# Optimization experiments

Hardware: AMD Instinct MI355X
Metric: run time of the kernel (lower is better)

## Reference

```python
import jax, jax.numpy as jnp
import numpy as np

B, N, E, H = 32, 1024, 1024, 8
D = E // H      # head_dim = 128, att_mid_dim = [128, 64, 128]
MID = 64


def setup_inputs() -> dict:
    key = jax.random.key(0)
    ks = jax.random.split(key, 12)

    def lin(k, out_d, in_d):
        return (jax.random.normal(k, (out_d, in_d), jnp.float32) * 0.02,
                jnp.zeros((out_d,), jnp.float32))

    Wq, bq = lin(ks[0], E, E)
    Wk, bk = lin(ks[1], E, E)
    Wv, bv = lin(ks[2], E, E)
    Wb, bb = lin(ks[3], MID, D)    # attention_basic: Linear(mid[0]=D -> mid[1]=64) + ReLU
    Wl, bl = lin(ks[4], 1, MID)    # attention_last: Linear(64 -> 1)
    Wl2, bl2 = lin(ks[5], D, MID)  # attention_last2: Linear(64 -> D)
    query = jax.random.normal(ks[6], (B, E), jnp.float32)
    k_in = jax.random.normal(ks[7], (B, N, E), jnp.float32)
    value1 = jax.random.normal(ks[8], (B, E), jnp.float32)
    value2 = jax.random.normal(ks[9], (B, N, E), jnp.float32)
    mask = jax.random.randint(ks[10], (B, N), 0, 2, jnp.int32)
    mask = mask.at[:, 0].set(1)  # guarantee at least one valid position per row
    return {"query": query, "key": k_in, "mask": mask, "value1": value1,
            "value2": value2, "Wq": Wq, "bq": bq, "Wk": Wk, "bk": bk,
            "Wv": Wv, "bv": bv, "Wb": Wb, "bb": bb, "Wl": Wl, "bl": bl,
            "Wl2": Wl2, "bl2": bl2}


def reference(query, key, mask, value1, value2, Wq, bq, Wk, bk, Wv, bv,
              Wb, bb, Wl, bl, Wl2, bl2):
    # --- QKV projections (single-query attention) ---
    Q = (query @ Wq.T + bq).reshape(B, 1, H, D).transpose(0, 2, 1, 3)    # [B,H,1,D]
    K = (key @ Wk.T + bk).reshape(B, N, H, D).transpose(0, 2, 1, 3)      # [B,H,N,D]
    V = (key @ Wv.T + bv).reshape(B, N, H, D).transpose(0, 2, 1, 3)      # [B,H,N,D]
    v1 = value1.reshape(B, H, D)                                          # [B,H,D]
    v2 = (value2 @ Wv.T + bv).reshape(B, N, H, D).transpose(0, 2, 1, 3)   # [B,H,N,D]

    scores = jnp.einsum('bhqd,bhkd->bhqk', Q, K) / jnp.sqrt(jnp.float32(D))  # [B,H,1,N]
    attended = jnp.einsum('bhqk,bhkd->bhqd', scores, V)                      # [B,H,1,D]
    attn_map = jnp.broadcast_to(attended, (B, H, N, D))                      # expand(-1,-1,N,-1)

    # --- SCAtt attn_net ---
    h = jax.nn.relu(jnp.einsum('bhnd,md->bhnm', attn_map, Wb) + bb)          # [B,H,N,64]
    mf = mask.astype(h.dtype)                                                # [B,N]
    mext = mf[:, None, :, None]                                              # [B,1,N,1]
    att_map_pool = jnp.sum(h * mext, axis=2) / jnp.sum(mext, axis=2)         # [B,H,64]
    alpha_spatial = (jnp.einsum('bhnm,om->bhno', h, Wl) + bl)[..., 0]        # [B,H,N]
    alpha_channel = jax.nn.sigmoid(att_map_pool @ Wl2.T + bl2)               # [B,H,D]
    alpha_spatial = jnp.where(mf[:, None, :] == 0, jnp.float32(-1e9), alpha_spatial)
    alpha_spatial = jax.nn.softmax(alpha_spatial, axis=-1)                   # [B,H,N]
    v2_att = jnp.einsum('bhn,bhnd->bhd', alpha_spatial, v2)                  # [B,H,D]
    attn = v1 * v2_att * alpha_channel                                       # [B,H,D]
    return attn.reshape(B, H * D)
```

## Files before the change

### kernel.cpp

```cpp
#include <hip/hip_runtime.h>

#define B_  32
#define N_  1024
#define E_  1024
#define H_  8
#define D_  128
#define MID_ 64
#define NT_  32
#define TR_  32
#define NSP_ 32


__global__ __launch_bounds__(256) void k_qkproj(
        const float* __restrict__ query, const float* __restrict__ Wq,
        const float* __restrict__ bq, const float* __restrict__ Wk,
        const float* __restrict__ bk, float* __restrict__ qk,
        float* __restrict__ qb)
{
    const int bh = blockIdx.x;
    const int b = bh >> 3, h = bh & 7;
    const int t = threadIdx.x;
    const int l = t & 63, w = t >> 6;
    const int rg = l >> 4, cl = l & 15;

    __shared__ __align__(16) float qsh[E_];
    __shared__ float Qs[D_];
    __shared__ float red[4];

    ((float4*)qsh)[t] = ((const float4*)(query + (size_t)b * E_))[t];
    __syncthreads();

    const float4* qsh4 = (const float4*)qsh;
    float qbacc = 0.f;
    #pragma unroll 2
    for (int p = 0; p < 8; ++p) {
        const int d = p * 16 + w * 4 + rg;
        const int row = h * D_ + d;
        const float4* wr = (const float4*)(Wq + (size_t)row * E_);
        float acc = 0.f;
        #pragma unroll 4
        for (int i = 0; i < 16; ++i) {
            float4 wv = wr[cl + i * 16];
            float4 qv = qsh4[cl + i * 16];
            acc += wv.x * qv.x + wv.y * qv.y + wv.z * qv.z + wv.w * qv.w;
        }
        #pragma unroll
        for (int off = 8; off; off >>= 1) acc += __shfl_xor(acc, off);
        if (cl == 0) {
            float q = acc + bq[row];
            Qs[d] = q;
            qbacc += q * bk[row];
        }
    }
    #pragma unroll
    for (int off = 32; off; off >>= 1) qbacc += __shfl_down(qbacc, off);
    if (l == 0) red[w] = qbacc;
    __syncthreads();
    if (t == 0) qb[bh] = red[0] + red[1] + red[2] + red[3];

    const int e0 = t * 4;
    float4 a = make_float4(0.f, 0.f, 0.f, 0.f);
    const float* wkb = Wk + (size_t)(h * D_) * E_ + e0;
    #pragma unroll 8
    for (int d = 0; d < D_; ++d) {
        float Qd = Qs[d];
        float4 wv = *(const float4*)(wkb + (size_t)d * E_);
        a.x += Qd * wv.x; a.y += Qd * wv.y; a.z += Qd * wv.z; a.w += Qd * wv.w;
    }
    *(float4*)(qk + (size_t)bh * E_ + e0) = a;
}

__global__ __launch_bounds__(256) void k_main(
        const float* __restrict__ key, const float* __restrict__ qk,
        const float* __restrict__ qb, float* __restrict__ PPpart,
        float* __restrict__ ssum,
        const float* __restrict__ value2, const int* __restrict__ mask,
        float* __restrict__ P2p)
{
    const int t = threadIdx.x;

    __shared__ __align__(16) float part[4][4][8];
    __shared__ __align__(16) float sfin[4][8];
    __shared__ int rows[NSP_];
    __shared__ int nrows;

    if ((blockIdx.x & 1) == 0) {
        const int si = blockIdx.x >> 1;
        const int tile = si & 31, b = si >> 5;
        const int w = t >> 6, l = t & 63;

        const float scale = 0.08838834764831845f;
        const float* keyb = key + ((size_t)b * N_ + (size_t)tile * TR_) * E_;
        const float qbv = (t < 32) ? qb[b * 8 + (t & 7)] : 0.f;

        float4 qkr[8];
        #pragma unroll
        for (int h = 0; h < H_; ++h)
            qkr[h] = ((const float4*)(qk + (size_t)(b * 8 + h) * E_))[t];

        float4 pacc[8];
        #pragma unroll
        for (int h = 0; h < 8; ++h) pacc[h] = make_float4(0.f, 0.f, 0.f, 0.f);

        float ts = 0.f;

        float4 kv[4];
        #pragma unroll
        for (int r = 0; r < 4; ++r)
            kv[r] = ((const float4*)(keyb + (size_t)r * E_))[t];

        for (int st = 0; st < 8; ++st) {
            #pragma unroll
            for (int r = 0; r < 4; ++r) {
                float p[8];
                #pragma unroll
                for (int h = 0; h < 8; ++h)
                    p[h] = qkr[h].x * kv[r].x + qkr[h].y * kv[r].y
                         + qkr[h].z * kv[r].z + qkr[h].w * kv[r].w;
                #pragma unroll
                for (int off = 32; off; off >>= 1) {
                    #pragma unroll
                    for (int h = 0; h < 8; ++h)
                        p[h] += __shfl_xor(p[h], off);
                }
                if (l == 0) {
                    *(float4*)&part[w][r][0] = make_float4(p[0], p[1], p[2], p[3]);
                    *(float4*)&part[w][r][4] = make_float4(p[4], p[5], p[6], p[7]);
                }
            }
            float4 kn[4];
            if (st < 7) {
                #pragma unroll
                for (int r = 0; r < 4; ++r)
                    kn[r] = ((const float4*)(keyb
                                + (size_t)((st + 1) * 4 + r) * E_))[t];
            }
            __syncthreads();
            if (t < 32) {
                const int r = t >> 3, h = t & 7;
                float s = (part[0][r][h] + part[1][r][h]
                         + part[2][r][h] + part[3][r][h] + qbv) * scale;
                sfin[r][h] = s;
                ts += s;
            }
            __syncthreads();
            #pragma unroll
            for (int r = 0; r < 4; ++r) {
                const float4 k4 = kv[r];
                const float4 sA = *(const float4*)&sfin[r][0];
                const float4 sB = *(const float4*)&sfin[r][4];
                pacc[0].x += sA.x * k4.x; pacc[0].y += sA.x * k4.y;
                pacc[0].z += sA.x * k4.z; pacc[0].w += sA.x * k4.w;
                pacc[1].x += sA.y * k4.x; pacc[1].y += sA.y * k4.y;
                pacc[1].z += sA.y * k4.z; pacc[1].w += sA.y * k4.w;
                pacc[2].x += sA.z * k4.x; pacc[2].y += sA.z * k4.y;
                pacc[2].z += sA.z * k4.z; pacc[2].w += sA.z * k4.w;
                pacc[3].x += sA.w * k4.x; pacc[3].y += sA.w * k4.y;
                pacc[3].z += sA.w * k4.z; pacc[3].w += sA.w * k4.w;
                pacc[4].x += sB.x * k4.x; pacc[4].y += sB.x * k4.y;
                pacc[4].z += sB.x * k4.z; pacc[4].w += sB.x * k4.w;
                pacc[5].x += sB.y * k4.x; pacc[5].y += sB.y * k4.y;
                pacc[5].z += sB.y * k4.z; pacc[5].w += sB.y * k4.w;
                pacc[6].x += sB.z * k4.x; pacc[6].y += sB.z * k4.y;
                pacc[6].z += sB.z * k4.z; pacc[6].w += sB.z * k4.w;
                pacc[7].x += sB.w * k4.x; pacc[7].y += sB.w * k4.y;
                pacc[7].z += sB.w * k4.z; pacc[7].w += sB.w * k4.w;
            }
            #pragma unroll
            for (int r = 0; r < 4; ++r) kv[r] = kn[r];
        }

        if (t < 32) {
            float v = ts;
            v += __shfl_xor(v, 8);
            v += __shfl_xor(v, 16);
            if (l < 8) atomicAdd(&ssum[b * 8 + l], v);
        }

        #pragma unroll
        for (int h = 0; h < 8; ++h) {
            ((float4*)(PPpart
                + (((size_t)(b * H_ + h)) * NT_ + tile) * E_))[t] = pacc[h];
        }
    } else {
        const int pi = blockIdx.x >> 1;
        const int b = pi & 31, sp = pi >> 5;
        const int e0 = t * 4;
        const int n0 = sp * NSP_;

        if (t == 0) nrows = 0;
        __syncthreads();
        if (t < NSP_) {
            if (mask[b * N_ + n0 + t]) {
                int i2 = atomicAdd(&nrows, 1);
                rows[i2] = t;
            }
        }
        __syncthreads();
        const int nr = nrows;

        float a0 = 0.f, a1 = 0.f, a2 = 0.f, a3 = 0.f;
        const float* vb = value2 + ((size_t)(b * N_ + n0)) * E_ + e0;
        #pragma unroll 4
        for (int i = 0; i < nr; ++i) {
            float4 v = *(const float4*)(vb + (size_t)rows[i] * E_);
            a0 += v.x; a1 += v.y; a2 += v.z; a3 += v.w;
        }
        float* dst = P2p + ((size_t)(sp & 7) * B_ + b) * E_ + e0;
        atomicAdd(dst + 0, a0); atomicAdd(dst + 1, a1);
        atomicAdd(dst + 2, a2); atomicAdd(dst + 3, a3);
    }
}

__global__ __launch_bounds__(512) void k_tail(
        const float* __restrict__ PPpart, const float* __restrict__ P2p,
        const float* __restrict__ ssumg, const int* __restrict__ mask,
        const float* __restrict__ Wv, const float* __restrict__ bv,
        const float* __restrict__ Wb, const float* __restrict__ bb,
        const float* __restrict__ Wl2, const float* __restrict__ bl2,
        const float* __restrict__ value1, float* __restrict__ out)
{
    const int bh = blockIdx.x, b = bh >> 3, h = bh & 7;
    const int t = threadIdx.x;
    const int l = t & 63, w = t >> 6;
    const int rg = l >> 4, cl = l & 15;

    __shared__ __align__(16) float ph[2][E_];
    __shared__ __align__(16) float pooled[E_];
    __shared__ __align__(16) float pool2[E_];
    __shared__ float attA_s[D_];
    __shared__ float attV_s[D_];
    __shared__ float att[D_];
    __shared__ float hv[MID_];
    __shared__ float red2[2];
    __shared__ float cnt_s;

    {
        const int c4 = t & 255, half = t >> 8;
        const float4* pp = (const float4*)(PPpart + (size_t)bh * NT_ * E_);
        float4 s = make_float4(0.f, 0.f, 0.f, 0.f);
        #pragma unroll 4
        for (int j = 0; j < 16; ++j) {
            float4 v = pp[(half * 16 + j) * 256 + c4];
            s.x += v.x; s.y += v.y; s.z += v.z; s.w += v.w;
        }
        ((float4*)&ph[half][0])[c4] = s;
    }
    __syncthreads();
    if (t < 256) {
        float4 p0 = ((const float4*)&ph[0][0])[t];
        float4 p1 = ((const float4*)&ph[1][0])[t];
        ((float4*)pooled)[t] = make_float4(p0.x + p1.x, p0.y + p1.y,
                                           p0.z + p1.z, p0.w + p1.w);
        float4 q = make_float4(0.f, 0.f, 0.f, 0.f);
        #pragma unroll
        for (int k2 = 0; k2 < 8; ++k2) {
            float4 v = ((const float4*)(P2p + ((size_t)k2 * B_ + b) * E_))[t];
            q.x += v.x; q.y += v.y; q.z += v.z; q.w += v.w;
        }
        ((float4*)pool2)[t] = q;
    }
    __syncthreads();

    const float4* pooled4 = (const float4*)pooled;
    const float4* pool24  = (const float4*)pool2;
    #pragma unroll
    for (int p = 0; p < 4; ++p) {
        const int d = p * 32 + w * 4 + rg;
        const float4* wvr = (const float4*)(Wv + (size_t)(h * D_ + d) * E_);
        float pA = 0.f, pV = 0.f;
        #pragma unroll 4
        for (int i = 0; i < 16; ++i) {
            float4 wv4 = wvr[cl + i * 16];
            float4 pa = pooled4[cl + i * 16];
            float4 pb = pool24[cl + i * 16];
            pA += wv4.x * pa.x + wv4.y * pa.y + wv4.z * pa.z + wv4.w * pa.w;
            pV += wv4.x * pb.x + wv4.y * pb.y + wv4.z * pb.z + wv4.w * pb.w;
        }
        #pragma unroll
        for (int off = 8; off; off >>= 1) {
            pA += __shfl_xor(pA, off);
            pV += __shfl_xor(pV, off);
        }
        if (cl == 0) { attA_s[d] = pA; attV_s[d] = pV; }
    }
    __syncthreads();

    if (t < 128) {
        int ci = 0;
        #pragma unroll
        for (int i = 0; i < 8; ++i) ci += mask[b * N_ + t + i * 128];
        float cf = (float)ci;
        #pragma unroll
        for (int off = 32; off; off >>= 1) cf += __shfl_down(cf, off);
        if ((t & 63) == 0) red2[t >> 6] = cf;
        const float ss = ssumg[bh];
        att[t] = attA_s[t] + ss * bv[h * D_ + t];
    }
    __syncthreads();
    if (t == 0) cnt_s = red2[0] + red2[1];
    if (t < MID_) {
        float a = bb[t];
        #pragma unroll 4
        for (int d2 = 0; d2 < D_; ++d2) a += att[d2] * Wb[t * D_ + d2];
        hv[t] = fmaxf(a, 0.f);
    }
    __syncthreads();
    if (t < 128) {
        float z = bl2[t];
        #pragma unroll
        for (int m = 0; m < MID_; ++m) z += hv[m] * Wl2[t * MID_ + m];
        float alphac = 1.f / (1.f + expf(-z));
        const float bvd = bv[h * D_ + t];
        float v2a = attV_s[t] / cnt_s + bvd;
        out[(size_t)b * E_ + h * D_ + t] =
            value1[(size_t)b * E_ + h * D_ + t] * v2a * alphac;
    }
}

extern "C" void kernel_launch(void* const* d_in, const int* in_sizes, int n_in,
                              void* d_out, int out_size, void* d_ws, size_t ws_size,
                              hipStream_t stream)
{
    const float* query  = (const float*)d_in[0];
    const float* key    = (const float*)d_in[1];
    const int*   mask   = (const int*)d_in[2];
    const float* value1 = (const float*)d_in[3];
    const float* value2 = (const float*)d_in[4];
    const float* Wq  = (const float*)d_in[5];
    const float* bq  = (const float*)d_in[6];
    const float* Wk  = (const float*)d_in[7];
    const float* bk  = (const float*)d_in[8];
    const float* Wv  = (const float*)d_in[9];
    const float* bv  = (const float*)d_in[10];
    const float* Wb  = (const float*)d_in[11];
    const float* bb  = (const float*)d_in[12];
    const float* Wl2 = (const float*)d_in[15];
    const float* bl2 = (const float*)d_in[16];
    float* out = (float*)d_out;

    char* ws = (char*)d_ws;
    const size_t SZ_PPP = (size_t)B_ * H_ * NT_ * E_ * 4;
    const size_t SZ_P2P = (size_t)8 * B_ * E_ * 4;
    const size_t OFF_P2P = SZ_PPP;
    const size_t OFF_SS  = OFF_P2P + SZ_P2P;
    const size_t OFF_QB  = OFF_SS + 1024;
    const size_t OFF_QK  = OFF_QB + 1024;
    float* PPpart = (float*)(ws);
    float* P2p  = (float*)(ws + OFF_P2P);
    float* ssum = (float*)(ws + OFF_SS);
    float* qb   = (float*)(ws + OFF_QB);
    float* qk   = (float*)(ws + OFF_QK);

    hipMemsetAsync(ws + OFF_P2P, 0, SZ_P2P + 1024, stream);

    hipLaunchKernelGGL(k_qkproj, dim3(B_ * H_), dim3(256), 0, stream,
                       query, Wq, bq, Wk, bk, qk, qb);
    hipLaunchKernelGGL(k_main, dim3(2 * NT_ * B_), dim3(256), 0, stream,
                       key, qk, qb, PPpart, ssum, value2, mask, P2p);
    hipLaunchKernelGGL(k_tail, dim3(B_ * H_), dim3(512), 0, stream,
                       PPpart, P2p, ssum, mask, Wv, bv, Wb, bb, Wl2, bl2,
                       value1, out);
}
```

Measured before the change: 437.5 us.

## Batch weight projections across batch rows and split pipeline into six kernels

The Q projection, the Wk projection, and the Wv projection in the tail now load each weight row once and reuse it across 8 or 32 batch elements, where before they streamed the weights separately for every (b,h) block. The value2 masked pooling moves out of k_main and runs alongside the Q projection, so k_main only handles the key tiles. The tail is split into a reduction kernel, a batched Wv matvec kernel and a small final kernel. This cuts redundant weight traffic (Wq, Wk and Wv were each read many times) at the cost of more kernel launches and extra global round trips for intermediates.

Result: faster. 371.7 us (-15.0%).

```diff
diff --git a/kernel.cpp b/kernel.cpp
--- a/kernel.cpp
+++ b/kernel.cpp
@@ -11,179 +11,73 @@
 #define NSP_ 32
 
 
-__global__ __launch_bounds__(256) void k_qkproj(
+__global__ __launch_bounds__(256) void k_q(
         const float* __restrict__ query, const float* __restrict__ Wq,
-        const float* __restrict__ bq, const float* __restrict__ Wk,
-        const float* __restrict__ bk, float* __restrict__ qk,
-        float* __restrict__ qb)
-{
-    const int bh = blockIdx.x;
-    const int b = bh >> 3, h = bh & 7;
-    const int t = threadIdx.x;
-    const int l = t & 63, w = t >> 6;
-    const int rg = l >> 4, cl = l & 15;
-
-    __shared__ __align__(16) float qsh[E_];
-    __shared__ float Qs[D_];
-    __shared__ float red[4];
-
-    ((float4*)qsh)[t] = ((const float4*)(query + (size_t)b * E_))[t];
-    __syncthreads();
-
-    const float4* qsh4 = (const float4*)qsh;
-    float qbacc = 0.f;
-    #pragma unroll 2
-    for (int p = 0; p < 8; ++p) {
-        const int d = p * 16 + w * 4 + rg;
-        const int row = h * D_ + d;
-        const float4* wr = (const float4*)(Wq + (size_t)row * E_);
-        float acc = 0.f;
-        #pragma unroll 4
-        for (int i = 0; i < 16; ++i) {
-            float4 wv = wr[cl + i * 16];
-            float4 qv = qsh4[cl + i * 16];
-            acc += wv.x * qv.x + wv.y * qv.y + wv.z * qv.z + wv.w * qv.w;
-        }
-        #pragma unroll
-        for (int off = 8; off; off >>= 1) acc += __shfl_xor(acc, off);
-        if (cl == 0) {
-            float q = acc + bq[row];
-            Qs[d] = q;
-            qbacc += q * bk[row];
-        }
-    }
-    #pragma unroll
-    for (int off = 32; off; off >>= 1) qbacc += __shfl_down(qbacc, off);
-    if (l == 0) red[w] = qbacc;
-    __syncthreads();
-    if (t == 0) qb[bh] = red[0] + red[1] + red[2] + red[3];
-
-    const int e0 = t * 4;
-    float4 a = make_float4(0.f, 0.f, 0.f, 0.f);
-    const float* wkb = Wk + (size_t)(h * D_) * E_ + e0;
-    #pragma unroll 8
-    for (int d = 0; d < D_; ++d) {
-        float Qd = Qs[d];
-        float4 wv = *(const float4*)(wkb + (size_t)d * E_);
-        a.x += Qd * wv.x; a.y += Qd * wv.y; a.z += Qd * wv.z; a.w += Qd * wv.w;
-    }
-    *(float4*)(qk + (size_t)bh * E_ + e0) = a;
-}
-
-__global__ __launch_bounds__(256) void k_main(
-        const float* __restrict__ key, const float* __restrict__ qk,
-        const float* __restrict__ qb, float* __restrict__ PPpart,
-        float* __restrict__ ssum,
+        const float* __restrict__ bq, const float* __restrict__ bk,
+        float* __restrict__ Qs, float* __restrict__ qb,
         const float* __restrict__ value2, const int* __restrict__ mask,
         float* __restrict__ P2p)
 {
     const int t = threadIdx.x;
 
-    __shared__ __align__(16) float part[4][4][8];
-    __shared__ __align__(16) float sfin[4][8];
+    __shared__ __align__(16) float qsh[8 * E_];
+    __shared__ __align__(16) float Qrow[8][16];
     __shared__ int rows[NSP_];
     __shared__ int nrows;
 
-    if ((blockIdx.x & 1) == 0) {
-        const int si = blockIdx.x >> 1;
-        const int tile = si & 31, b = si >> 5;
-        const int w = t >> 6, l = t & 63;
-
-        const float scale = 0.08838834764831845f;
-        const float* keyb = key + ((size_t)b * N_ + (size_t)tile * TR_) * E_;
-        const float qbv = (t < 32) ? qb[b * 8 + (t & 7)] : 0.f;
-
-        float4 qkr[8];
-        #pragma unroll
-        for (int h = 0; h < H_; ++h)
-            qkr[h] = ((const float4*)(qk + (size_t)(b * 8 + h) * E_))[t];
-
-        float4 pacc[8];
-        #pragma unroll
-        for (int h = 0; h < 8; ++h) pacc[h] = make_float4(0.f, 0.f, 0.f, 0.f);
-
-        float ts = 0.f;
-
-        float4 kv[4];
-        #pragma unroll
-        for (int r = 0; r < 4; ++r)
-            kv[r] = ((const float4*)(keyb + (size_t)r * E_))[t];
-
-        for (int st = 0; st < 8; ++st) {
-            #pragma unroll
-            for (int r = 0; r < 4; ++r) {
-                float p[8];
-                #pragma unroll
-                for (int h = 0; h < 8; ++h)
-                    p[h] = qkr[h].x * kv[r].x + qkr[h].y * kv[r].y
-                         + qkr[h].z * kv[r].z + qkr[h].w * kv[r].w;
-                #pragma unroll
-                for (int off = 32; off; off >>= 1) {
-                    #pragma unroll
-                    for (int h = 0; h < 8; ++h)
-                        p[h] += __shfl_xor(p[h], off);
-                }
-                if (l == 0) {
-                    *(float4*)&part[w][r][0] = make_float4(p[0], p[1], p[2], p[3]);
-                    *(float4*)&part[w][r][4] = make_float4(p[4], p[5], p[6], p[7]);
-                }
+    if (blockIdx.x < 256) {
+        const int bg = blockIdx.x >> 6;
+        const int rs = blockIdx.x & 63;
+        const int b0 = bg * 8;
+        const int R  = rs * 16;
+        const int h  = rs >> 3;
+
+        {
+            const int bb = t >> 5, ln = t & 31;
+            const float4* src = (const float4*)(query + (size_t)(b0 + bb) * E_);
+            float4* dst = (float4*)(qsh + bb * E_);
+            #pragma unroll
+            for (int i = 0; i < 8; ++i) dst[ln + i * 32] = src[ln + i * 32];
+        }
+        __syncthreads();
+
+        const int r = t >> 4, cl = t & 15;
+        const int row = R + r;
+        const float4* wr = (const float4*)(Wq + (size_t)row * E_);
+        float4 wchunk[16];
+        #pragma unroll
+        for (int i = 0; i < 16; ++i) wchunk[i] = wr[cl + i * 16];
+
+        const float bqv = bq[row];
+        const float4* qsh4 = (const float4*)qsh;
+        #pragma unroll
+        for (int bb = 0; bb < 8; ++bb) {
+            float acc = 0.f;
+            #pragma unroll
+            for (int i = 0; i < 16; ++i) {
+                float4 q = qsh4[bb * 256 + cl + i * 16];
+                acc += wchunk[i].x * q.x + wchunk[i].y * q.y
+                     + wchunk[i].z * q.z + wchunk[i].w * q.w;
             }
-            float4 kn[4];
-            if (st < 7) {
-                #pragma unroll
-                for (int r = 0; r < 4; ++r)
-                    kn[r] = ((const float4*)(keyb
-                                + (size_t)((st + 1) * 4 + r) * E_))[t];
-            }
-            __syncthreads();
-            if (t < 32) {
-                const int r = t >> 3, h = t & 7;
-                float s = (part[0][r][h] + part[1][r][h]
-                         + part[2][r][h] + part[3][r][h] + qbv) * scale;
-                sfin[r][h] = s;
-                ts += s;
-            }
-            __syncthreads();
-            #pragma unroll
-            for (int r = 0; r < 4; ++r) {
-                const float4 k4 = kv[r];
-                const float4 sA = *(const float4*)&sfin[r][0];
-                const float4 sB = *(const float4*)&sfin[r][4];
-                pacc[0].x += sA.x * k4.x; pacc[0].y += sA.x * k4.y;
-                pacc[0].z += sA.x * k4.z; pacc[0].w += sA.x * k4.w;
-                pacc[1].x += sA.y * k4.x; pacc[1].y += sA.y * k4.y;
-                pacc[1].z += sA.y * k4.z; pacc[1].w += sA.y * k4.w;
-                pacc[2].x += sA.z * k4.x; pacc[2].y += sA.z * k4.y;
-                pacc[2].z += sA.z * k4.z; pacc[2].w += sA.z * k4.w;
-                pacc[3].x += sA.w * k4.x; pacc[3].y += sA.w * k4.y;
-                pacc[3].z += sA.w * k4.z; pacc[3].w += sA.w * k4.w;
-                pacc[4].x += sB.x * k4.x; pacc[4].y += sB.x * k4.y;
-                pacc[4].z += sB.x * k4.z; pacc[4].w += sB.x * k4.w;
-                pacc[5].x += sB.y * k4.x; pacc[5].y += sB.y * k4.y;
-                pacc[5].z += sB.y * k4.z; pacc[5].w += sB.y * k4.w;
-                pacc[6].x += sB.z * k4.x; pacc[6].y += sB.z * k4.y;
-                pacc[6].z += sB.z * k4.z; pacc[6].w += sB.z * k4.w;
-                pacc[7].x += sB.w * k4.x; pacc[7].y += sB.w * k4.y;
-                pacc[7].z += sB.w * k4.z; pacc[7].w += sB.w * k4.w;
-            }
-            #pragma unroll
-            for (int r = 0; r < 4; ++r) kv[r] = kn[r];
-        }
-
+            #pragma unroll
+            for (int off = 8; off; off >>= 1) acc += __shfl_xor(acc, off);
+            if (cl == 0) Qrow[bb][r] = acc + bqv;
+        }
+        __syncthreads();
+
+        if (t < 8) {
+            float s = 0.f;
+            #pragma unroll
+            for (int rr = 0; rr < 16; ++rr) s += Qrow[t][rr] * bk[R + rr];
+            atomicAdd(&qb[(b0 + t) * 8 + h], s);
+        }
         if (t < 32) {
-            float v = ts;
-            v += __shfl_xor(v, 8);
-            v += __shfl_xor(v, 16);
-            if (l < 8) atomicAdd(&ssum[b * 8 + l], v);
-        }
-
-        #pragma unroll
-        for (int h = 0; h < 8; ++h) {
-            ((float4*)(PPpart
-                + (((size_t)(b * H_ + h)) * NT_ + tile) * E_))[t] = pacc[h];
+            const int bb = t >> 2, j = t & 3;
+            ((float4*)(Qs + (size_t)(b0 + bb) * E_))[rs * 4 + j] =
+                *(const float4*)&Qrow[bb][j * 4];
         }
     } else {
-        const int pi = blockIdx.x >> 1;
+        const int pi = blockIdx.x - 256;
         const int b = pi & 31, sp = pi >> 5;
         const int e0 = t * 4;
         const int n0 = sp * NSP_;
@@ -212,91 +106,271 @@
     }
 }
 
-__global__ __launch_bounds__(512) void k_tail(
+__global__ __launch_bounds__(256) void k_k(
+        const float* __restrict__ Qs, const float* __restrict__ Wk,
+        float* __restrict__ qk)
+{
+    const int h = blockIdx.x >> 5, ec = blockIdx.x & 31;
+    const int t = threadIdx.x;
+
+    __shared__ __align__(16) float QsL[32 * 132];
+    __shared__ __align__(16) float WkL[128 * 32];
+
+    {
+        const int b = t >> 3, j = t & 7;
+        const float4* src = (const float4*)(Qs + (size_t)b * E_) + h * 32;
+        float4* dst = (float4*)(QsL + b * 132);
+        #pragma unroll
+        for (int jj = 0; jj < 4; ++jj) dst[j + jj * 8] = src[j + jj * 8];
+    }
+    {
+        #pragma unroll
+        for (int jj = 0; jj < 4; ++jj) {
+            const int idx = t + jj * 256;
+            const int d = idx >> 3, c = idx & 7;
+            ((float4*)WkL)[idx] =
+                ((const float4*)(Wk + (size_t)(h * D_ + d) * E_))[ec * 8 + c];
+        }
+    }
+    __syncthreads();
+
+    const int b = t >> 3, eg = t & 7;
+    float4 acc = make_float4(0.f, 0.f, 0.f, 0.f);
+    const float* q = QsL + b * 132;
+    const float4* wk4 = (const float4*)WkL;
+    #pragma unroll 8
+    for (int d = 0; d < D_; ++d) {
+        float qd = q[d];
+        float4 w = wk4[d * 8 + eg];
+        acc.x += qd * w.x; acc.y += qd * w.y;
+        acc.z += qd * w.z; acc.w += qd * w.w;
+    }
+    ((float4*)(qk + (size_t)(b * 8 + h) * E_))[ec * 8 + eg] = acc;
+}
+
+__global__ __launch_bounds__(256) void k_main(
+        const float* __restrict__ key, const float* __restrict__ qk,
+        const float* __restrict__ qb, float* __restrict__ PPpart,
+        float* __restrict__ ssum)
+{
+    const int tile = blockIdx.x, b = blockIdx.y;
+    const int t = threadIdx.x;
+    const int w = t >> 6, l = t & 63;
+
+    __shared__ __align__(16) float part[4][4][8];
+    __shared__ __align__(16) float sfin[4][8];
+
+    const float scale = 0.08838834764831845f;
+    const float* keyb = key + ((size_t)b * N_ + (size_t)tile * TR_) * E_;
+    const float qbv = (t < 32) ? qb[b * 8 + (t & 7)] : 0.f;
+
+    float4 qkr[8];
+    #pragma unroll
+    for (int h = 0; h < H_; ++h)
+        qkr[h] = ((const float4*)(qk + (size_t)(b * 8 + h) * E_))[t];
+
+    float4 pacc[8];
+    #pragma unroll
+    for (int h = 0; h < 8; ++h) pacc[h] = make_float4(0.f, 0.f, 0.f, 0.f);
+
+    float ts = 0.f;
+
+    float4 kv[4];
+    #pragma unroll
+    for (int r = 0; r < 4; ++r)
+        kv[r] = ((const float4*)(keyb + (size_t)r * E_))[t];
+
+    for (int st = 0; st < 8; ++st) {
+        #pragma unroll
+        for (int r = 0; r < 4; ++r) {
+            float p[8];
+            #pragma unroll
+            for (int h = 0; h < 8; ++h)
+                p[h] = qkr[h].x * kv[r].x + qkr[h].y * kv[r].y
+                     + qkr[h].z * kv[r].z + qkr[h].w * kv[r].w;
+            #pragma unroll
+            for (int off = 32; off; off >>= 1) {
+                #pragma unroll
+                for (int h = 0; h < 8; ++h)
+                    p[h] += __shfl_xor(p[h], off);
+            }
+            if (l == 0) {
+                *(float4*)&part[w][r][0] = make_float4(p[0], p[1], p[2], p[3]);
+                *(float4*)&part[w][r][4] = make_float4(p[4], p[5], p[6], p[7]);
+            }
+        }
+        float4 kn[4];
+        if (st < 7) {
+            #pragma unroll
+            for (int r = 0; r < 4; ++r)
+                kn[r] = ((const float4*)(keyb
+                            + (size_t)((st + 1) * 4 + r) * E_))[t];
+        }
+        __syncthreads();
+        if (t < 32) {
+            const int r = t >> 3, h = t & 7;
+            float s = (part[0][r][h] + part[1][r][h]
+                     + part[2][r][h] + part[3][r][h] + qbv) * scale;
+            sfin[r][h] = s;
+            ts += s;
+        }
+        __syncthreads();
+        #pragma unroll
+        for (int r = 0; r < 4; ++r) {
+            const float4 k4 = kv[r];
+            const float4 sA = *(const float4*)&sfin[r][0];
+            const float4 sB = *(const float4*)&sfin[r][4];
+            pacc[0].x += sA.x * k4.x; pacc[0].y += sA.x * k4.y;
+            pacc[0].z += sA.x * k4.z; pacc[0].w += sA.x * k4.w;
+            pacc[1].x += sA.y * k4.x; pacc[1].y += sA.y * k4.y;
+            pacc[1].z += sA.y * k4.z; pacc[1].w += sA.y * k4.w;
+            pacc[2].x += sA.z * k4.x; pacc[2].y += sA.z * k4.y;
+            pacc[2].z += sA.z * k4.z; pacc[2].w += sA.z * k4.w;
+            pacc[3].x += sA.w * k4.x; pacc[3].y += sA.w * k4.y;
+            pacc[3].z += sA.w * k4.z; pacc[3].w += sA.w * k4.w;
+            pacc[4].x += sB.x * k4.x; pacc[4].y += sB.x * k4.y;
+            pacc[4].z += sB.x * k4.z; pacc[4].w += sB.x * k4.w;
+            pacc[5].x += sB.y * k4.x; pacc[5].y += sB.y * k4.y;
+            pacc[5].z += sB.y * k4.z; pacc[5].w += sB.y * k4.w;
+            pacc[6].x += sB.z * k4.x; pacc[6].y += sB.z * k4.y;
+            pacc[6].z += sB.z * k4.z; pacc[6].w += sB.z * k4.w;
+            pacc[7].x += sB.w * k4.x; pacc[7].y += sB.w * k4.y;
+            pacc[7].z += sB.w * k4.z; pacc[7].w += sB.w * k4.w;
+        }
+        #pragma unroll
+        for (int r = 0; r < 4; ++r) kv[r] = kn[r];
+    }
+
+    if (t < 32) {
+        float v = ts;
+        v += __shfl_xor(v, 8);
+        v += __shfl_xor(v, 16);
+        if (l < 8) atomicAdd(&ssum[b * 8 + l], v);
+    }
+
+    #pragma unroll
+    for (int h = 0; h < 8; ++h) {
+        ((float4*)(PPpart
+            + (((size_t)(b * H_ + h)) * NT_ + tile) * E_))[t] = pacc[h];
+    }
+}
+
+__global__ __launch_bounds__(256) void k_red(
         const float* __restrict__ PPpart, const float* __restrict__ P2p,
+        float* __restrict__ pooled, float* __restrict__ pool2)
+{
+    const int bh = blockIdx.x;
+    const int t = threadIdx.x;
+    const float4* pp = (const float4*)(PPpart + (size_t)bh * NT_ * E_);
+    float4 s = make_float4(0.f, 0.f, 0.f, 0.f);
+    #pragma unroll 8
+    for (int tl = 0; tl < NT_; ++tl) {
+        float4 v = pp[tl * 256 + t];
+        s.x += v.x; s.y += v.y; s.z += v.z; s.w += v.w;
+    }
+    ((float4*)(pooled + (size_t)bh * E_))[t] = s;
+
+    if (bh < B_) {
+        float4 q = make_float4(0.f, 0.f, 0.f, 0.f);
+        #pragma unroll
+        for (int k2 = 0; k2 < 8; ++k2) {
+            float4 v = ((const float4*)(P2p + ((size_t)k2 * B_ + bh) * E_))[t];
+            q.x += v.x; q.y += v.y; q.z += v.z; q.w += v.w;
+        }
+        ((float4*)(pool2 + (size_t)bh * E_))[t] = q;
+    }
+}
+
+__global__ __launch_bounds__(256) void k_att2(
+        const float* __restrict__ pooled, const float* __restrict__ pool2,
+        const float* __restrict__ Wv,
+        float* __restrict__ attA, float* __restrict__ attV)
+{
+    const int h  = blockIdx.x >> 5;
+    const int dc = (blockIdx.x >> 2) & 7;
+    const int bq = blockIdx.x & 3;
+    const int t = threadIdx.x;
+
+    __shared__ __align__(16) float pL[8 * E_];
+    __shared__ __align__(16) float p2L[8 * E_];
+
+    {
+        const int bb = t >> 5, ln = t & 31;
+        const int b = bq * 8 + bb;
+        const float4* sp = (const float4*)(pooled + (size_t)(b * 8 + h) * E_);
+        const float4* s2 = (const float4*)(pool2 + (size_t)b * E_);
+        float4* dp = (float4*)(pL + bb * E_);
+        float4* d2 = (float4*)(p2L + bb * E_);
+        #pragma unroll
+        for (int i = 0; i < 8; ++i) {
+            dp[ln + i * 32] = sp[ln + i * 32];
+            d2[ln + i * 32] = s2[ln + i * 32];
+        }
+    }
+    __syncthreads();
+
+    const int r = t >> 4, cl = t & 15;
+    const int d = dc * 16 + r;
+    const float4* wvr = (const float4*)(Wv + (size_t)(h * D_ + d) * E_);
+    const float4* pL4 = (const float4*)pL;
+    const float4* p2L4 = (const float4*)p2L;
+
+    float aA[8] = {}, aV[8] = {};
+    #pragma unroll 4
+    for (int i = 0; i < 16; ++i) {
+        float4 w = wvr[cl + i * 16];
+        #pragma unroll
+        for (int bb = 0; bb < 8; ++bb) {
+            float4 pa = pL4[bb * 256 + cl + i * 16];
+            float4 pb = p2L4[bb * 256 + cl + i * 16];
+            aA[bb] += w.x * pa.x + w.y * pa.y + w.z * pa.z + w.w * pa.w;
+            aV[bb] += w.x * pb.x + w.y * pb.y + w.z * pb.z + w.w * pb.w;
+        }
+    }
+    #pragma unroll
+    for (int off = 8; off; off >>= 1) {
+        #pragma unroll
+        for (int bb = 0; bb < 8; ++bb) {
+            aA[bb] += __shfl_xor(aA[bb], off);
+            aV[bb] += __shfl_xor(aV[bb], off);
+        }
+    }
+    if (cl == 0) {
+        #pragma unroll
+        for (int bb = 0; bb < 8; ++bb) {
+            const int bh = (bq * 8 + bb) * 8 + h;
+            attA[(size_t)bh * D_ + d] = aA[bb];
+            attV[(size_t)bh * D_ + d] = aV[bb];
+        }
+    }
+}
+
+__global__ __launch_bounds__(128) void k_final(
+        const float* __restrict__ attA, const float* __restrict__ attV,
         const float* __restrict__ ssumg, const int* __restrict__ mask,
-        const float* __restrict__ Wv, const float* __restrict__ bv,
-        const float* __restrict__ Wb, const float* __restrict__ bb,
-        const float* __restrict__ Wl2, const float* __restrict__ bl2,
-        const float* __restrict__ value1, float* __restrict__ out)
+        const float* __restrict__ bv, const float* __restrict__ Wb,
+        const float* __restrict__ bb, const float* __restrict__ Wl2,
+        const float* __restrict__ bl2, const float* __restrict__ value1,
+        float* __restrict__ out)
 {
     const int bh = blockIdx.x, b = bh >> 3, h = bh & 7;
     const int t = threadIdx.x;
-    const int l = t & 63, w = t >> 6;
-    const int rg = l >> 4, cl = l & 15;
-
-    __shared__ __align__(16) float ph[2][E_];
-    __shared__ __align__(16) float pooled[E_];
-    __shared__ __align__(16) float pool2[E_];
-    __shared__ float attA_s[D_];
-    __shared__ float attV_s[D_];
+
     __shared__ float att[D_];
     __shared__ float hv[MID_];
     __shared__ float red2[2];
     __shared__ float cnt_s;
 
-    {
-        const int c4 = t & 255, half = t >> 8;
-        const float4* pp = (const float4*)(PPpart + (size_t)bh * NT_ * E_);
-        float4 s = make_float4(0.f, 0.f, 0.f, 0.f);
-        #pragma unroll 4
-        for (int j = 0; j < 16; ++j) {
-            float4 v = pp[(half * 16 + j) * 256 + c4];
-            s.x += v.x; s.y += v.y; s.z += v.z; s.w += v.w;
-        }
-        ((float4*)&ph[half][0])[c4] = s;
-    }
-    __syncthreads();
-    if (t < 256) {
-        float4 p0 = ((const float4*)&ph[0][0])[t];
-        float4 p1 = ((const float4*)&ph[1][0])[t];
-        ((float4*)pooled)[t] = make_float4(p0.x + p1.x, p0.y + p1.y,
-                                           p0.z + p1.z, p0.w + p1.w);
-        float4 q = make_float4(0.f, 0.f, 0.f, 0.f);
-        #pragma unroll
-        for (int k2 = 0; k2 < 8; ++k2) {
-            float4 v = ((const float4*)(P2p + ((size_t)k2 * B_ + b) * E_))[t];
-            q.x += v.x; q.y += v.y; q.z += v.z; q.w += v.w;
-        }
-        ((float4*)pool2)[t] = q;
-    }
-    __syncthreads();
-
-    const float4* pooled4 = (const float4*)pooled;
-    const float4* pool24  = (const float4*)pool2;
-    #pragma unroll
-    for (int p = 0; p < 4; ++p) {
-        const int d = p * 32 + w * 4 + rg;
-        const float4* wvr = (const float4*)(Wv + (size_t)(h * D_ + d) * E_);
-        float pA = 0.f, pV = 0.f;
-        #pragma unroll 4
-        for (int i = 0; i < 16; ++i) {
-            float4 wv4 = wvr[cl + i * 16];
-            float4 pa = pooled4[cl + i * 16];
-            float4 pb = pool24[cl + i * 16];
-            pA += wv4.x * pa.x + wv4.y * pa.y + wv4.z * pa.z + wv4.w * pa.w;
-            pV += wv4.x * pb.x + wv4.y * pb.y + wv4.z * pb.z + wv4.w * pb.w;
-        }
-        #pragma unroll
-        for (int off = 8; off; off >>= 1) {
-            pA += __shfl_xor(pA, off);
-            pV += __shfl_xor(pV, off);
-        }
-        if (cl == 0) { attA_s[d] = pA; attV_s[d] = pV; }
-    }
-    __syncthreads();
-
-    if (t < 128) {
-        int ci = 0;
-        #pragma unroll
-        for (int i = 0; i < 8; ++i) ci += mask[b * N_ + t + i * 128];
-        float cf = (float)ci;
-        #pragma unroll
-        for (int off = 32; off; off >>= 1) cf += __shfl_down(cf, off);
-        if ((t & 63) == 0) red2[t >> 6] = cf;
-        const float ss = ssumg[bh];
-        att[t] = attA_s[t] + ss * bv[h * D_ + t];
-    }
+    int ci = 0;
+    #pragma unroll
+    for (int i = 0; i < 8; ++i) ci += mask[b * N_ + t + i * 128];
+    float cf = (float)ci;
+    #pragma unroll
+    for (int off = 32; off; off >>= 1) cf += __shfl_down(cf, off);
+    if ((t & 63) == 0) red2[t >> 6] = cf;
+
+    const float ss = ssumg[bh];
+    att[t] = attA[(size_t)bh * D_ + t] + ss * bv[h * D_ + t];
     __syncthreads();
     if (t == 0) cnt_s = red2[0] + red2[1];
     if (t < MID_) {
@@ -306,16 +380,15 @@
         hv[t] = fmaxf(a, 0.f);
     }
     __syncthreads();
-    if (t < 128) {
-        float z = bl2[t];
-        #pragma unroll
-        for (int m = 0; m < MID_; ++m) z += hv[m] * Wl2[t * MID_ + m];
-        float alphac = 1.f / (1.f + expf(-z));
-        const float bvd = bv[h * D_ + t];
-        float v2a = attV_s[t] / cnt_s + bvd;
-        out[(size_t)b * E_ + h * D_ + t] =
-            value1[(size_t)b * E_ + h * D_ + t] * v2a * alphac;
-    }
+
+    float z = bl2[t];
+    #pragma unroll
+    for (int m = 0; m < MID_; ++m) z += hv[m] * Wl2[t * MID_ + m];
+    float alphac = 1.f / (1.f + expf(-z));
+    const float bvd = bv[h * D_ + t];
+    float v2a = attV[(size_t)bh * D_ + t] / cnt_s + bvd;
+    out[(size_t)b * E_ + h * D_ + t] =
+        value1[(size_t)b * E_ + h * D_ + t] * v2a * alphac;
 }
 
 extern "C" void kernel_launch(void* const* d_in, const int* in_sizes, int n_in,
@@ -345,20 +418,36 @@
     const size_t OFF_P2P = SZ_PPP;
     const size_t OFF_SS  = OFF_P2P + SZ_P2P;
     const size_t OFF_QB  = OFF_SS + 1024;
-    const size_t OFF_QK  = OFF_QB + 1024;
+    const size_t OFF_QS  = OFF_QB + 1024;
+    const size_t OFF_QK  = OFF_QS + (size_t)B_ * E_ * 4;
+    const size_t OFF_PL  = OFF_QK + (size_t)B_ * H_ * E_ * 4;
+    const size_t OFF_P2  = OFF_PL + (size_t)B_ * H_ * E_ * 4;
+    const size_t OFF_AA  = OFF_P2 + (size_t)B_ * E_ * 4;
+    const size_t OFF_AV  = OFF_AA + (size_t)B_ * H_ * D_ * 4;
     float* PPpart = (float*)(ws);
-    float* P2p  = (float*)(ws + OFF_P2P);
-    float* ssum = (float*)(ws + OFF_SS);
-    float* qb   = (float*)(ws + OFF_QB);
-    float* qk   = (float*)(ws + OFF_QK);
-
-    hipMemsetAsync(ws + OFF_P2P, 0, SZ_P2P + 1024, stream);
-
-    hipLaunchKernelGGL(k_qkproj, dim3(B_ * H_), dim3(256), 0, stream,
-                       query, Wq, bq, Wk, bk, qk, qb);
-    hipLaunchKernelGGL(k_main, dim3(2 * NT_ * B_), dim3(256), 0, stream,
-                       key, qk, qb, PPpart, ssum, value2, mask, P2p);
-    hipLaunchKernelGGL(k_tail, dim3(B_ * H_), dim3(512), 0, stream,
-                       PPpart, P2p, ssum, mask, Wv, bv, Wb, bb, Wl2, bl2,
+    float* P2p    = (float*)(ws + OFF_P2P);
+    float* ssum   = (float*)(ws + OFF_SS);
+    float* qb     = (float*)(ws + OFF_QB);
+    float* Qs     = (float*)(ws + OFF_QS);
+    float* qk     = (float*)(ws + OFF_QK);
+    float* pooled = (float*)(ws + OFF_PL);
+    float* pool2  = (float*)(ws + OFF_P2);
+    float* attA   = (float*)(ws + OFF_AA);
+    float* attV   = (float*)(ws + OFF_AV);
+
+    hipMemsetAsync(ws + OFF_P2P, 0, SZ_P2P + 2048, stream);
+
+    hipLaunchKernelGGL(k_q, dim3(256 + NT_ * B_), dim3(256), 0, stream,
+                       query, Wq, bq, bk, Qs, qb, value2, mask, P2p);
+    hipLaunchKernelGGL(k_k, dim3(256), dim3(256), 0, stream,
+                       Qs, Wk, qk);
+    hipLaunchKernelGGL(k_main, dim3(NT_, B_), dim3(256), 0, stream,
+                       key, qk, qb, PPpart, ssum);
+    hipLaunchKernelGGL(k_red, dim3(B_ * H_), dim3(256), 0, stream,
+                       PPpart, P2p, pooled, pool2);
+    hipLaunchKernelGGL(k_att2, dim3(256), dim3(256), 0, stream,
+                       pooled, pool2, Wv, attA, attV);
+    hipLaunchKernelGGL(k_final, dim3(B_ * H_), dim3(128), 0, stream,
+                       attA, attV, ssum, mask, bv, Wb, bb, Wl2, bl2,
                        value1, out);
 }
```
